# Optimization experiments

Measured on AMD Instinct MI355X. Metric: run time of the kernel, lower is better.

The kernel has to match this reference:

```python
import jax, jax.numpy as jnp
import numpy as np

COORD_DIM = 2
ENTITY_DIM = 1024
FIELD_DIM = 512
INPUT_DIM = 512
NUM_ENTITIES = 512
FIELD_RESOLUTION = 10000  # grid_size = 100


def _gelu(x):
    return jax.nn.gelu(x, approximate=False)  # torch nn.GELU default (erf)


def setup_inputs() -> dict:
    key = jax.random.key(0)
    ks = jax.random.split(key, 9)
    std = 0.02  # matches _init_parameters
    B, S = 8, 4096
    x = jax.random.normal(ks[0], (B, S, INPUT_DIM), dtype=jnp.float32)
    # DensityField: density_projection = Linear(D,F) GELU Linear(F,F) GELU; coordinate_generator = Linear(F,2)
    W1 = jax.random.normal(ks[1], (INPUT_DIM, FIELD_DIM), jnp.float32) * std
    b1 = jnp.zeros((FIELD_DIM,), jnp.float32)
    W2 = jax.random.normal(ks[2], (FIELD_DIM, FIELD_DIM), jnp.float32) * std
    b2 = jnp.zeros((FIELD_DIM,), jnp.float32)
    Wc = jax.random.normal(ks[3], (FIELD_DIM, COORD_DIM), jnp.float32) * std
    bc = jnp.zeros((COORD_DIM,), jnp.float32)
    # entity_mapper: Linear(F+2, F) GELU Linear(F, E+2+1)
    We1 = jax.random.normal(ks[4], (FIELD_DIM + COORD_DIM, FIELD_DIM), jnp.float32) * std
    be1 = jnp.zeros((FIELD_DIM,), jnp.float32)
    We2 = jax.random.normal(ks[5], (FIELD_DIM, ENTITY_DIM + COORD_DIM + 1), jnp.float32) * std
    be2 = jnp.zeros((ENTITY_DIM + COORD_DIM + 1,), jnp.float32)
    # output_projection: Linear(E, 2E) GELU Linear(2E, D)
    Wo1 = jax.random.normal(ks[6], (ENTITY_DIM, 2 * ENTITY_DIM), jnp.float32) * std
    bo1 = jnp.zeros((2 * ENTITY_DIM,), jnp.float32)
    Wo2 = jax.random.normal(ks[7], (2 * ENTITY_DIM, INPUT_DIM), jnp.float32) * std
    bo2 = jnp.zeros((INPUT_DIM,), jnp.float32)
    return dict(x=x, W1=W1, b1=b1, W2=W2, b2=b2, Wc=Wc, bc=bc,
                We1=We1, be1=be1, We2=We2, be2=be2,
                Wo1=Wo1, bo1=bo1, Wo2=Wo2, bo2=bo2)


def _forward(x, W1, b1, W2, b2, Wc, bc, We1, be1, We2, be2, Wo1, bo1, Wo2, bo2):
    # --- DensityField ---
    df = _gelu(_gelu(x @ W1 + b1) @ W2 + b2)          # [B,S,F]
    coords = df @ Wc + bc                              # [B,S,2]
    # --- ContinuousEntityExtractor ---
    field_input = jnp.concatenate([coords, df], axis=-1)          # [B,S,2+F]
    ef = _gelu(field_input @ We1 + be1) @ We2 + be2                # [B,S,E+3]
    importance = jnp.linalg.norm(ef, axis=-1)                      # [B,S]
    _, top_idx = jax.lax.top_k(importance, NUM_ENTITIES)           # [B,Ne]
    sel = jnp.take_along_axis(ef, top_idx[..., None], axis=1)     # [B,Ne,E+3]
    positions = sel[..., :COORD_DIM]                               # [B,Ne,2]
    states = sel[..., COORD_DIM:COORD_DIM + ENTITY_DIM]            # [B,Ne,E]
    # --- ContinuousOutputGenerator ---
    proj = _gelu(states @ Wo1 + bo1) @ Wo2 + bo2                   # [B,Ne,D]
    grid_size = int(FIELD_RESOLUTION ** 0.5)
    g = jnp.linspace(-1.0, 1.0, grid_size)
    gx, gy = jnp.meshgrid(g, g, indexing='ij')
    grid = jnp.stack([gx.ravel(), gy.ravel()], axis=-1)            # [G2,2]
    # squared euclidean distances via expansion (torch: cdist then **2)
    g2 = jnp.sum(grid * grid, axis=-1)                             # [G2]
    p2 = jnp.sum(positions * positions, axis=-1)                   # [B,Ne]
    gp = jnp.einsum('gc,bnc->bgn', grid, positions)                # [B,G2,Ne]
    sq = g2[None, :, None] + p2[:, None, :] - 2.0 * gp             # [B,G2,Ne]
    attn = jnp.exp(-sq / 0.1)
    attn = attn / (attn.sum(axis=-1, keepdims=True) + 1e-8)
    out = jnp.einsum('bgn,bnd->bgd', attn, proj)                   # [B,G2,D]
    return out


def reference(x, W1, b1, W2, b2, Wc, bc, We1, be1, We2, be2, Wo1, bo1, Wo2, bo2):
    return _forward(x, W1, b1, W2, b2, Wc, bc, We1, be1, We2, be2, Wo1, bo1, Wo2, bo2)
```

## Files before the change

kernel.cpp:

```cpp
#include <hip/hip_runtime.h>
#include <hip/hip_bf16.h>
#include <math.h>


typedef __attribute__((ext_vector_type(8))) short bf16x8;
typedef __attribute__((ext_vector_type(4))) float f32x4;

__device__ __forceinline__ float gelu_exact(float x) {
    return 0.5f * x * (1.0f + erff(x * 0.7071067811865476f));
}

__device__ __forceinline__ void async_copy16(const void* g, void* l) {
    __builtin_amdgcn_global_load_lds(
        (const __attribute__((address_space(1))) unsigned int*)g,
        (__attribute__((address_space(3))) unsigned int*)l, 16, 0, 0);
}

__global__ __launch_bounds__(256) void split_kernel(
    const float* __restrict__ in,
    __hip_bfloat16* __restrict__ hi, __hip_bfloat16* __restrict__ lo)
{
    const int i4 = blockIdx.x * 256 + threadIdx.x;
    const float4 v = ((const float4*)in)[i4];
    __hip_bfloat16 h0 = __float2bfloat16(v.x);
    __hip_bfloat16 h1 = __float2bfloat16(v.y);
    __hip_bfloat16 h2 = __float2bfloat16(v.z);
    __hip_bfloat16 h3 = __float2bfloat16(v.w);
    __hip_bfloat16 l0 = __float2bfloat16(v.x - __bfloat162float(h0));
    __hip_bfloat16 l1 = __float2bfloat16(v.y - __bfloat162float(h1));
    __hip_bfloat16 l2 = __float2bfloat16(v.z - __bfloat162float(h2));
    __hip_bfloat16 l3 = __float2bfloat16(v.w - __bfloat162float(h3));
    union { __hip_bfloat16 h[4]; short4 s; } uh, ul;
    uh.h[0] = h0; uh.h[1] = h1; uh.h[2] = h2; uh.h[3] = h3;
    ul.h[0] = l0; ul.h[1] = l1; ul.h[2] = l2; ul.h[3] = l3;
    ((short4*)hi)[i4] = uh.s;
    ((short4*)lo)[i4] = ul.s;
}

__global__ __launch_bounds__(256) void transpose_split_kernel(
    const float* __restrict__ in,
    __hip_bfloat16* __restrict__ outH, __hip_bfloat16* __restrict__ outL,
    int K, int N)
{
    __shared__ float tile[32][33];
    const int k0 = blockIdx.y * 32, n0 = blockIdx.x * 32;
    const int t = threadIdx.x;
    const int lr = t >> 5, lc = t & 31;
    #pragma unroll
    for (int p = 0; p < 4; p++) {
        const int r = p * 8 + lr;
        const int n = n0 + lc;
        tile[r][lc] = (n < N) ? in[(size_t)(k0 + r) * N + n] : 0.f;
    }
    __syncthreads();
    #pragma unroll
    for (int p = 0; p < 4; p++) {
        const int r = p * 8 + lr;
        const float v = tile[lc][r];
        const __hip_bfloat16 h = __float2bfloat16(v);
        const __hip_bfloat16 l = __float2bfloat16(v - __bfloat162float(h));
        outH[(size_t)(n0 + r) * K + k0 + lc] = h;
        outL[(size_t)(n0 + r) * K + k0 + lc] = l;
    }
}

__global__ __launch_bounds__(256) void init_kernel(
    float* __restrict__ IMP, float* __restrict__ CRD,
    const float* __restrict__ bc)
{
    const int t = blockIdx.x * 256 + threadIdx.x;
    IMP[t] = 0.f;
    ((float2*)CRD)[t] = make_float2(bc[0], bc[1]);
}

template<bool GELU, bool RANK2, bool EFMODE, bool FUSEC>
__global__ __launch_bounds__(256) void gemm3k(
    const __hip_bfloat16* __restrict__ Ahi, const __hip_bfloat16* __restrict__ Alo,
    const __hip_bfloat16* __restrict__ Bhi, const __hip_bfloat16* __restrict__ Blo,
    const float* __restrict__ bias,
    __hip_bfloat16* __restrict__ Chi, __hip_bfloat16* __restrict__ Clo,
    __hip_bfloat16* __restrict__ EFB, float* __restrict__ EFC,
    float* __restrict__ IMP,
    const float* __restrict__ A2, const float* __restrict__ W2r,
    float* __restrict__ CRD, const float* __restrict__ Wc)
{
    __shared__ __align__(16) __hip_bfloat16 AsH[4096];
    __shared__ __align__(16) __hip_bfloat16 AsL[4096];
    __shared__ __align__(16) __hip_bfloat16 BsH[4096];
    __shared__ __align__(16) __hip_bfloat16 BsL[4096];
    const int t = threadIdx.x;
    const int wave = t >> 6, lane = t & 63;
    const int wave_m = wave >> 1, wave_n = wave & 1;
    const int fr = lane & 15, quad = lane >> 4;
    const int gx = gridDim.x;
    const int L = blockIdx.y * gx + blockIdx.x;
    const int xcd = L & 7, kk_ = L >> 3;
    const int m_blk = xcd * (gridDim.y >> 3) + kk_ / gx;
    const int n_blk = kk_ % gx;
    const int m0 = m_blk * 128;
    const int n0 = n_blk * 128;
    const int lrow   = lane & 15;
    const int lchunk = (lane >> 4) * 8;

    f32x4 acc[4][4] = {};

    const int abase = wave_m * 2048 + quad * 128 + fr * 8;
    const int bbase = wave_n * 2048 + quad * 128 + fr * 8;

    for (int step = 0; step < 16; ++step) {
        const int kk = step << 5;
        #pragma unroll
        for (int s = 0; s < 2; s++) {
            const int seg = wave * 2 + s;
            const size_t ao = (size_t)(m0 + seg * 16 + lrow) * 512 + kk + lchunk;
            const size_t bo = (size_t)(n0 + seg * 16 + lrow) * 512 + kk + lchunk;
            async_copy16(Ahi + ao, &AsH[seg * 512]);
            async_copy16(Alo + ao, &AsL[seg * 512]);
            async_copy16(Bhi + bo, &BsH[seg * 512]);
            async_copy16(Blo + bo, &BsL[seg * 512]);
        }
        __syncthreads();
        bf16x8 ah[4], al[4], bh[4], bl[4];
        #pragma unroll
        for (int i = 0; i < 4; i++) {
            ah[i] = *(const bf16x8*)&AsH[abase + i * 512];
            al[i] = *(const bf16x8*)&AsL[abase + i * 512];
        }
        #pragma unroll
        for (int j = 0; j < 4; j++) {
            bh[j] = *(const bf16x8*)&BsH[bbase + j * 512];
            bl[j] = *(const bf16x8*)&BsL[bbase + j * 512];
        }
        #pragma unroll
        for (int i = 0; i < 4; i++)
            #pragma unroll
            for (int j = 0; j < 4; j++)
                acc[i][j] = __builtin_amdgcn_mfma_f32_16x16x32_bf16(
                    ah[i], bh[j], acc[i][j], 0, 0, 0);
        #pragma unroll
        for (int i = 0; i < 4; i++)
            #pragma unroll
            for (int j = 0; j < 4; j++)
                acc[i][j] = __builtin_amdgcn_mfma_f32_16x16x32_bf16(
                    ah[i], bl[j], acc[i][j], 0, 0, 0);
        #pragma unroll
        for (int i = 0; i < 4; i++)
            #pragma unroll
            for (int j = 0; j < 4; j++)
                acc[i][j] = __builtin_amdgcn_mfma_f32_16x16x32_bf16(
                    al[i], bh[j], acc[i][j], 0, 0, 0);
        __syncthreads();
    }

    #pragma unroll
    for (int i = 0; i < 4; i++) {
        const int gmb = m0 + wave_m * 64 + i * 16 + quad * 4;
        float a2x[4], a2y[4];
        if (RANK2) {
            #pragma unroll
            for (int r = 0; r < 4; r++) {
                a2x[r] = A2[(size_t)(gmb + r) * 2];
                a2y[r] = A2[(size_t)(gmb + r) * 2 + 1];
            }
        }
        float f0[4] = {0.f, 0.f, 0.f, 0.f};
        float f1[4] = {0.f, 0.f, 0.f, 0.f};
        #pragma unroll
        for (int j = 0; j < 4; j++) {
            const int gn = n0 + wave_n * 64 + j * 16 + fr;
            const bool nok = !EFMODE || (gn < 1027);
            const float bv = nok ? bias[gn] : 0.f;
            float w2a = 0.f, w2b = 0.f;
            if (RANK2) { w2a = W2r[gn]; w2b = W2r[512 + gn]; }
            float wcx = 0.f, wcy = 0.f;
            if (FUSEC) {
                const float2 wc = ((const float2*)Wc)[gn];
                wcx = wc.x; wcy = wc.y;
            }
            #pragma unroll
            for (int r = 0; r < 4; r++) {
                const int gm = gmb + r;
                float v = acc[i][j][r] + bv;
                if (RANK2) v += a2x[r] * w2a + a2y[r] * w2b;
                if (GELU) v = gelu_exact(v);
                if (EFMODE) {
                    if (gn < 2) EFC[(size_t)gm * 2 + gn] = v;
                    else if (gn < 1026)
                        EFB[(size_t)gm * 1024 + gn - 2] = __float2bfloat16(v);
                    if (nok) f0[r] += v * v;
                } else {
                    const __hip_bfloat16 h = __float2bfloat16(v);
                    const __hip_bfloat16 l =
                        __float2bfloat16(v - __bfloat162float(h));
                    Chi[(size_t)gm * 512 + gn] = h;
                    Clo[(size_t)gm * 512 + gn] = l;
                    if (FUSEC) { f0[r] += v * wcx; f1[r] += v * wcy; }
                }
            }
        }
        if (EFMODE || FUSEC) {
            #pragma unroll
            for (int r = 0; r < 4; r++) {
                float a = f0[r], b = f1[r];
                #pragma unroll
                for (int off = 1; off < 16; off <<= 1) {
                    a += __shfl_xor(a, off);
                    if (FUSEC) b += __shfl_xor(b, off);
                }
                if (fr == 0) {
                    if (FUSEC) {
                        atomicAdd(&CRD[(size_t)(gmb + r) * 2],     a);
                        atomicAdd(&CRD[(size_t)(gmb + r) * 2 + 1], b);
                    } else {
                        atomicAdd(&IMP[gmb + r], a);
                    }
                }
            }
        }
    }
}

__global__ __launch_bounds__(1024) void topk_kernel(
    const float* __restrict__ IMP, int* __restrict__ IDX)
{
    __shared__ float v[4096];
    __shared__ int   ix[4096];
    const int b = blockIdx.x, t = threadIdx.x;
    for (int i = t; i < 4096; i += 1024) {
        v[i] = sqrtf(IMP[b * 4096 + i]);
        ix[i] = i;
    }
    __syncthreads();
    for (int k = 2; k <= 4096; k <<= 1) {
        for (int j = k >> 1; j > 0; j >>= 1) {
            for (int q = 0; q < 4; q++) {
                const int i = t + (q << 10);
                const int l = i ^ j;
                if (l > i) {
                    const float vi = v[i], vl = v[l];
                    const int   ii = ix[i], il = ix[l];
                    const bool after = (vi < vl) || (vi == vl && ii > il);
                    const bool dirAsc = ((i & k) == 0);
                    if (dirAsc ? after : !after) {
                        v[i] = vl; v[l] = vi; ix[i] = il; ix[l] = ii;
                    }
                }
            }
            __syncthreads();
        }
    }
    if (t < 512) IDX[b * 512 + t] = ix[t];
}

__global__ __launch_bounds__(256) void gather_kernel(
    const __hip_bfloat16* __restrict__ EFB, const float* __restrict__ EFC,
    const int* __restrict__ IDX,
    float* __restrict__ POS, __hip_bfloat16* __restrict__ ST)
{
    const int bn  = blockIdx.x;
    const int b   = bn >> 9;
    const int row = IDX[bn];
    const size_t src = (size_t)(b * 4096) + row;
    const int t = threadIdx.x;
    if (t < 2) POS[(size_t)bn * 2 + t] = EFC[src * 2 + t];
    const unsigned int* s = (const unsigned int*)(EFB + src * 1024);
    unsigned int* d = (unsigned int*)(ST + (size_t)bn * 1024);
    d[t]       = s[t];
    d[t + 256] = s[t + 256];
}

__global__ __launch_bounds__(256) void transpose_cvt_kernel(
    const float* __restrict__ in, __hip_bfloat16* __restrict__ out,
    int K, int N)
{
    __shared__ float tile[32][33];
    const int k0 = blockIdx.y * 32, n0 = blockIdx.x * 32;
    const int t = threadIdx.x;
    const int lr = t >> 5, lc = t & 31;
    #pragma unroll
    for (int p = 0; p < 4; p++) {
        const int r = p * 8 + lr;
        tile[r][lc] = in[(size_t)(k0 + r) * N + n0 + lc];
    }
    __syncthreads();
    #pragma unroll
    for (int p = 0; p < 4; p++) {
        const int r = p * 8 + lr;
        out[(size_t)(n0 + r) * K + k0 + lc] = __float2bfloat16(tile[lc][r]);
    }
}

__global__ __launch_bounds__(256) void transpose_proj_kernel(
    const __hip_bfloat16* __restrict__ in, __hip_bfloat16* __restrict__ out)
{
    __shared__ __hip_bfloat16 tile[32][33];
    const int b = blockIdx.z;
    const int n0 = blockIdx.y * 32, d0 = blockIdx.x * 32;
    const int t = threadIdx.x;
    const int lr = t >> 5, lc = t & 31;
    #pragma unroll
    for (int p = 0; p < 4; p++) {
        const int r = p * 8 + lr;
        tile[r][lc] = in[((size_t)b * 512 + n0 + r) * 512 + d0 + lc];
    }
    __syncthreads();
    #pragma unroll
    for (int p = 0; p < 4; p++) {
        const int r = p * 8 + lr;
        out[((size_t)b * 512 + d0 + r) * 512 + n0 + lc] = tile[lc][r];
    }
}

template<bool GELU>
__global__ __launch_bounds__(256, 4) void gemm_post(
    const __hip_bfloat16* __restrict__ A,
    const __hip_bfloat16* __restrict__ BT,
    const float* __restrict__ bias,
    __hip_bfloat16* __restrict__ C,
    int N, int K)
{
    __shared__ __align__(16) __hip_bfloat16 As[2][128][32];
    __shared__ __align__(16) __hip_bfloat16 Bs[2][128][32];
    const int t = threadIdx.x;
    const int wave = t >> 6, lane = t & 63;
    const int wave_m = wave >> 1, wave_n = wave & 1;
    const int fr = lane & 15, quad = lane >> 4;
    const int gx = gridDim.x;
    const int nwg = gx * gridDim.y;
    int lid = blockIdx.y * gx + blockIdx.x;
    {
        const int chunk = nwg >> 3;
        lid = (lid & 7) * chunk + (lid >> 3);
    }
    const int m0 = (lid / gx) * 128;
    const int n0 = (lid % gx) * 128;
    const int srow = lane >> 2;
    const int skc  = (lane & 3) * 8;
    const int nsteps = K >> 5;

    f32x4 acc[4][4] = {};

    auto STAGE = [&](int buf, int step) {
        const int kk = step << 5;
        #pragma unroll
        for (int s = 0; s < 2; s++) {
            const int seg = wave * 2 + s;
            const int row = seg * 16 + srow;
            async_copy16(A  + (size_t)(m0 + row) * K + kk + skc,
                         &As[buf][seg * 16][0]);
            async_copy16(BT + (size_t)(n0 + row) * K + kk + skc,
                         &Bs[buf][seg * 16][0]);
        }
    };

    STAGE(0, 0);
    __syncthreads();
    int cur = 0;
    for (int step = 0; step < nsteps; ++step) {
        if (step + 1 < nsteps) STAGE(cur ^ 1, step + 1);
        bf16x8 af[4], bfv[4];
        #pragma unroll
        for (int i = 0; i < 4; i++)
            af[i] = *(const bf16x8*)&As[cur][wave_m * 64 + i * 16 + fr][quad * 8];
        #pragma unroll
        for (int j = 0; j < 4; j++)
            bfv[j] = *(const bf16x8*)&Bs[cur][wave_n * 64 + j * 16 + fr][quad * 8];
        #pragma unroll
        for (int i = 0; i < 4; i++)
            #pragma unroll
            for (int j = 0; j < 4; j++)
                acc[i][j] = __builtin_amdgcn_mfma_f32_16x16x32_bf16(
                    af[i], bfv[j], acc[i][j], 0, 0, 0);
        __syncthreads();
        cur ^= 1;
    }
    #pragma unroll
    for (int i = 0; i < 4; i++) {
        const int gm = m0 + wave_m * 64 + i * 16 + quad * 4;
        #pragma unroll
        for (int j = 0; j < 4; j++) {
            const int gn = n0 + wave_n * 64 + j * 16 + fr;
            const float bv = bias[gn];
            #pragma unroll
            for (int r = 0; r < 4; r++) {
                float v = acc[i][j][r] + bv;
                if (GELU) v = gelu_exact(v);
                C[(size_t)(gm + r) * N + gn] = __float2bfloat16(v);
            }
        }
    }
}

__global__ __launch_bounds__(256) void attn_mfma_kernel(
    const float* __restrict__ POS,
    const __hip_bfloat16* __restrict__ PROJT,
    float* __restrict__ OUT)
{
    __shared__ __align__(16) __hip_bfloat16 Bs[256][32];
    __shared__ float2 pos_s[512];
    __shared__ float srow_s[4][16];
    const int t = threadIdx.x;
    const int wave = t >> 6, lane = t & 63;
    const int fr = lane & 15, quad = lane >> 4;
    const int b  = blockIdx.z;
    const int g0 = blockIdx.x * 64;
    const int d0 = blockIdx.y * 256;

    {
        const float2* p = (const float2*)(POS + (size_t)b * 512 * 2);
        pos_s[t]       = p[t];
        pos_s[256 + t] = p[256 + t];
    }
    const int g = g0 + wave * 16 + fr;
    const bool gv = g < 10000;
    const float step = 2.0f / 99.0f;
    const int gi = gv ? (g / 100) : 0;
    const int gj = gv ? (g - gi * 100) : 0;
    const float gx = -1.f + step * (float)gi;
    const float gy = -1.f + step * (float)gj;

    f32x4 acc[16] = {};
    float wsum = 0.f;
    __syncthreads();

    for (int n0 = 0; n0 < 512; n0 += 32) {
        #pragma unroll
        for (int s = 0; s < 4; s++) {
            const int seg = wave * 4 + s;
            const __hip_bfloat16* gB = PROJT
                + ((size_t)b * 512 + d0 + seg * 16 + (lane >> 2)) * 512
                + n0 + (lane & 3) * 8;
            async_copy16(gB, &Bs[seg * 16][0]);
        }
        bf16x8 wf;
        float wl = 0.f;
        #pragma unroll
        for (int j = 0; j < 8; j++) {
            const int n = n0 + quad * 8 + j;
            const float2 pn = pos_s[n];
            const float dx = gx - pn.x, dy = gy - pn.y;
            const float w = gv ? __expf(-10.0f * (dx * dx + dy * dy)) : 0.f;
            const __hip_bfloat16 wb = __float2bfloat16(w);
            union { __hip_bfloat16 h; short s; } u; u.h = wb;
            wf[j] = u.s;
            wl += __bfloat162float(wb);
        }
        wsum += wl;
        __syncthreads();
        #pragma unroll
        for (int j = 0; j < 16; j++) {
            const bf16x8 bv = *(const bf16x8*)&Bs[j * 16 + fr][quad * 8];
            acc[j] = __builtin_amdgcn_mfma_f32_16x16x32_bf16(wf, bv, acc[j], 0, 0, 0);
        }
        __syncthreads();
    }
    wsum += __shfl_xor(wsum, 16);
    wsum += __shfl_xor(wsum, 32);
    if (lane < 16) srow_s[wave][lane] = wsum;
    __syncthreads();
    const int rbase = quad * 4;
    float inv[4];
    #pragma unroll
    for (int r = 0; r < 4; r++)
        inv[r] = 1.0f / (srow_s[wave][rbase + r] + 1e-8f);
    #pragma unroll
    for (int j = 0; j < 16; j++) {
        const int col = d0 + j * 16 + fr;
        #pragma unroll
        for (int r = 0; r < 4; r++) {
            const int gr = g0 + wave * 16 + rbase + r;
            if (gr < 10000)
                OUT[((size_t)b * 10000 + gr) * 512 + col] = acc[j][r] * inv[r];
        }
    }
}

extern "C" void kernel_launch(void* const* d_in, const int* in_sizes, int n_in,
                              void* d_out, int out_size, void* d_ws, size_t ws_size,
                              hipStream_t stream)
{
    const float* x   = (const float*)d_in[0];
    const float* W1  = (const float*)d_in[1];
    const float* b1  = (const float*)d_in[2];
    const float* W2  = (const float*)d_in[3];
    const float* b2  = (const float*)d_in[4];
    const float* Wc  = (const float*)d_in[5];
    const float* bc  = (const float*)d_in[6];
    const float* We1 = (const float*)d_in[7];
    const float* be1 = (const float*)d_in[8];
    const float* We2 = (const float*)d_in[9];
    const float* be2 = (const float*)d_in[10];
    const float* Wo1 = (const float*)d_in[11];
    const float* bo1 = (const float*)d_in[12];
    const float* Wo2 = (const float*)d_in[13];
    const float* bo2 = (const float*)d_in[14];
    float* out = (float*)d_out;

    const size_t BS = 32768;
    const size_t ACT = BS * 512;
    __hip_bfloat16* P0h = (__hip_bfloat16*)d_ws;
    __hip_bfloat16* P0l = P0h + ACT;
    __hip_bfloat16* P1h = P0l + ACT;
    __hip_bfloat16* P1l = P1h + ACT;
    __hip_bfloat16* EFB = P1l + ACT;
    float* EFC = (float*)(EFB + BS * 1024);
    float* CRD = EFC + BS * 2;
    float* IMP = CRD + BS * 2;
    int*   IDX = (int*)(IMP + BS);
    float* POS = (float*)(IDX + 4096);
    __hip_bfloat16* W1Th = (__hip_bfloat16*)(POS + 4096 * 2);
    __hip_bfloat16* W1Tl = W1Th + 512 * 512;
    __hip_bfloat16* W2Th = W1Tl + 512 * 512;
    __hip_bfloat16* W2Tl = W2Th + 512 * 512;
    __hip_bfloat16* We1Th = W2Tl + 512 * 512;
    __hip_bfloat16* We1Tl = We1Th + 512 * 512;
    __hip_bfloat16* We2Th = We1Tl + 512 * 512;
    __hip_bfloat16* We2Tl = We2Th + (size_t)1152 * 512;
    __hip_bfloat16* ST    = P0h;
    __hip_bfloat16* H4    = ST + (size_t)4096 * 1024;
    __hip_bfloat16* PROJ  = H4 + (size_t)4096 * 2048;
    __hip_bfloat16* PROJT = PROJ + (size_t)4096 * 512;
    __hip_bfloat16* Wo1T  = PROJT + (size_t)4096 * 512;
    __hip_bfloat16* Wo2T  = Wo1T + (size_t)2048 * 1024;

    dim3 blk(256);
    split_kernel<<<dim3(16384), blk, 0, stream>>>(x, P0h, P0l);
    transpose_split_kernel<<<dim3(16, 16), blk, 0, stream>>>(W1, W1Th, W1Tl, 512, 512);
    transpose_split_kernel<<<dim3(16, 16), blk, 0, stream>>>(W2, W2Th, W2Tl, 512, 512);
    transpose_split_kernel<<<dim3(16, 16), blk, 0, stream>>>(We1 + 2 * 512, We1Th, We1Tl, 512, 512);
    transpose_split_kernel<<<dim3(36, 16), blk, 0, stream>>>(We2, We2Th, We2Tl, 512, 1027);
    init_kernel<<<dim3(128), blk, 0, stream>>>(IMP, CRD, bc);
    gemm3k<true, false, false, false><<<dim3(4, 256), blk, 0, stream>>>(
        P0h, P0l, W1Th, W1Tl, b1, P1h, P1l,
        nullptr, nullptr, nullptr, nullptr, nullptr, nullptr, nullptr);
    gemm3k<true, false, false, true><<<dim3(4, 256), blk, 0, stream>>>(
        P1h, P1l, W2Th, W2Tl, b2, P0h, P0l,
        nullptr, nullptr, nullptr, nullptr, nullptr, CRD, Wc);
    gemm3k<true, true, false, false><<<dim3(4, 256), blk, 0, stream>>>(
        P0h, P0l, We1Th, We1Tl, be1, P1h, P1l,
        nullptr, nullptr, nullptr, CRD, We1, nullptr, nullptr);
    gemm3k<false, false, true, false><<<dim3(9, 256), blk, 0, stream>>>(
        P1h, P1l, We2Th, We2Tl, be2, nullptr, nullptr,
        EFB, EFC, IMP, nullptr, nullptr, nullptr, nullptr);
    topk_kernel<<<dim3(8), dim3(1024), 0, stream>>>(IMP, IDX);
    transpose_cvt_kernel<<<dim3(64, 32), blk, 0, stream>>>(Wo1, Wo1T, 1024, 2048);
    transpose_cvt_kernel<<<dim3(16, 64), blk, 0, stream>>>(Wo2, Wo2T, 2048, 512);
    gather_kernel<<<dim3(4096), blk, 0, stream>>>(EFB, EFC, IDX, POS, ST);
    gemm_post<true><<<dim3(16, 32), blk, 0, stream>>>(
        ST, Wo1T, bo1, H4, 2048, 1024);
    gemm_post<false><<<dim3(4, 32), blk, 0, stream>>>(
        H4, Wo2T, bo2, PROJ, 512, 2048);
    transpose_proj_kernel<<<dim3(16, 16, 8), blk, 0, stream>>>(PROJ, PROJT);
    attn_mfma_kernel<<<dim3(157, 2, 8), blk, 0, stream>>>(POS, PROJT, out);
}
```

Before: 941.9 us.

## Restructure GEMM kernels: drop XCD swizzle, store EF as fp32, split wrappers

Turns the templated GEMM into a device body with one named wrapper kernel per stage, and replaces the XCD-aware block remapping with a plain blockIdx mapping. The shared-memory staging moves to a row-major [128][32] tile with a different lane-to-row load pattern. The entity-feature output is now stored as a full fp32 1027-wide row instead of split bf16/fp32 buffers, and the gather kernel converts to bf16 itself. This doubles the EF write traffic. The row-major LDS reads may also cause bank conflicts, and dropping the swizzle loses L2 locality, so the change looks more like a simplification than a speedup.

```diff
diff --git a/kernel.cpp b/kernel.cpp
--- a/kernel.cpp
+++ b/kernel.cpp
@@ -73,63 +73,56 @@
     ((float2*)CRD)[t] = make_float2(bc[0], bc[1]);
 }
 
-template<bool GELU, bool RANK2, bool EFMODE, bool FUSEC>
-__global__ __launch_bounds__(256) void gemm3k(
+template<bool GELU, bool RANK2, bool SPLIT, bool FUSEC, bool FUSEI>
+__device__ __forceinline__ void gemm3k_body(
     const __hip_bfloat16* __restrict__ Ahi, const __hip_bfloat16* __restrict__ Alo,
     const __hip_bfloat16* __restrict__ Bhi, const __hip_bfloat16* __restrict__ Blo,
     const float* __restrict__ bias,
+    float* __restrict__ Cf, int ldc,
     __hip_bfloat16* __restrict__ Chi, __hip_bfloat16* __restrict__ Clo,
-    __hip_bfloat16* __restrict__ EFB, float* __restrict__ EFC,
-    float* __restrict__ IMP,
+    int N,
     const float* __restrict__ A2, const float* __restrict__ W2r,
-    float* __restrict__ CRD, const float* __restrict__ Wc)
-{
-    __shared__ __align__(16) __hip_bfloat16 AsH[4096];
-    __shared__ __align__(16) __hip_bfloat16 AsL[4096];
-    __shared__ __align__(16) __hip_bfloat16 BsH[4096];
-    __shared__ __align__(16) __hip_bfloat16 BsL[4096];
+    float* __restrict__ CRD, const float* __restrict__ Wc,
+    float* __restrict__ IMP)
+{
+    __shared__ __align__(16) __hip_bfloat16 AsH[128][32];
+    __shared__ __align__(16) __hip_bfloat16 AsL[128][32];
+    __shared__ __align__(16) __hip_bfloat16 BsH[128][32];
+    __shared__ __align__(16) __hip_bfloat16 BsL[128][32];
     const int t = threadIdx.x;
     const int wave = t >> 6, lane = t & 63;
     const int wave_m = wave >> 1, wave_n = wave & 1;
     const int fr = lane & 15, quad = lane >> 4;
-    const int gx = gridDim.x;
-    const int L = blockIdx.y * gx + blockIdx.x;
-    const int xcd = L & 7, kk_ = L >> 3;
-    const int m_blk = xcd * (gridDim.y >> 3) + kk_ / gx;
-    const int n_blk = kk_ % gx;
-    const int m0 = m_blk * 128;
-    const int n0 = n_blk * 128;
-    const int lrow   = lane & 15;
-    const int lchunk = (lane >> 4) * 8;
+    const int m0 = blockIdx.y * 128;
+    const int n0 = blockIdx.x * 128;
+    const int srow = lane >> 2;
+    const int skc  = (lane & 3) * 8;
 
     f32x4 acc[4][4] = {};
 
-    const int abase = wave_m * 2048 + quad * 128 + fr * 8;
-    const int bbase = wave_n * 2048 + quad * 128 + fr * 8;
-
-    for (int step = 0; step < 16; ++step) {
-        const int kk = step << 5;
+    for (int k0 = 0; k0 < 512; k0 += 32) {
         #pragma unroll
         for (int s = 0; s < 2; s++) {
             const int seg = wave * 2 + s;
-            const size_t ao = (size_t)(m0 + seg * 16 + lrow) * 512 + kk + lchunk;
-            const size_t bo = (size_t)(n0 + seg * 16 + lrow) * 512 + kk + lchunk;
-            async_copy16(Ahi + ao, &AsH[seg * 512]);
-            async_copy16(Alo + ao, &AsL[seg * 512]);
-            async_copy16(Bhi + bo, &BsH[seg * 512]);
-            async_copy16(Blo + bo, &BsL[seg * 512]);
+            const int row = seg * 16 + srow;
+            const size_t ao = (size_t)(m0 + row) * 512 + k0 + skc;
+            const size_t bo = (size_t)(n0 + row) * 512 + k0 + skc;
+            async_copy16(Ahi + ao, &AsH[seg * 16][0]);
+            async_copy16(Alo + ao, &AsL[seg * 16][0]);
+            async_copy16(Bhi + bo, &BsH[seg * 16][0]);
+            async_copy16(Blo + bo, &BsL[seg * 16][0]);
         }
         __syncthreads();
         bf16x8 ah[4], al[4], bh[4], bl[4];
         #pragma unroll
         for (int i = 0; i < 4; i++) {
-            ah[i] = *(const bf16x8*)&AsH[abase + i * 512];
-            al[i] = *(const bf16x8*)&AsL[abase + i * 512];
+            ah[i] = *(const bf16x8*)&AsH[wave_m * 64 + i * 16 + fr][quad * 8];
+            al[i] = *(const bf16x8*)&AsL[wave_m * 64 + i * 16 + fr][quad * 8];
         }
         #pragma unroll
         for (int j = 0; j < 4; j++) {
-            bh[j] = *(const bf16x8*)&BsH[bbase + j * 512];
-            bl[j] = *(const bf16x8*)&BsL[bbase + j * 512];
+            bh[j] = *(const bf16x8*)&BsH[wave_n * 64 + j * 16 + fr][quad * 8];
+            bl[j] = *(const bf16x8*)&BsL[wave_n * 64 + j * 16 + fr][quad * 8];
         }
         #pragma unroll
         for (int i = 0; i < 4; i++)
@@ -168,7 +161,7 @@
         #pragma unroll
         for (int j = 0; j < 4; j++) {
             const int gn = n0 + wave_n * 64 + j * 16 + fr;
-            const bool nok = !EFMODE || (gn < 1027);
+            const bool nok = SPLIT || (gn < N);
             const float bv = nok ? bias[gn] : 0.f;
             float w2a = 0.f, w2b = 0.f;
             if (RANK2) { w2a = W2r[gn]; w2b = W2r[512 + gn]; }
@@ -183,22 +176,20 @@
                 float v = acc[i][j][r] + bv;
                 if (RANK2) v += a2x[r] * w2a + a2y[r] * w2b;
                 if (GELU) v = gelu_exact(v);
-                if (EFMODE) {
-                    if (gn < 2) EFC[(size_t)gm * 2 + gn] = v;
-                    else if (gn < 1026)
-                        EFB[(size_t)gm * 1024 + gn - 2] = __float2bfloat16(v);
-                    if (nok) f0[r] += v * v;
-                } else {
+                if (SPLIT) {
                     const __hip_bfloat16 h = __float2bfloat16(v);
                     const __hip_bfloat16 l =
                         __float2bfloat16(v - __bfloat162float(h));
                     Chi[(size_t)gm * 512 + gn] = h;
                     Clo[(size_t)gm * 512 + gn] = l;
-                    if (FUSEC) { f0[r] += v * wcx; f1[r] += v * wcy; }
+                } else if (nok) {
+                    Cf[(size_t)gm * ldc + gn] = v;
                 }
+                if (FUSEC) { f0[r] += v * wcx; f1[r] += v * wcy; }
+                if (FUSEI && nok) f0[r] += v * v;
             }
         }
-        if (EFMODE || FUSEC) {
+        if (FUSEC || FUSEI) {
             #pragma unroll
             for (int r = 0; r < 4; r++) {
                 float a = f0[r], b = f1[r];
@@ -220,6 +211,52 @@
     }
 }
 
+__global__ __launch_bounds__(256) void gemm_h1(
+    const __hip_bfloat16* __restrict__ Ahi, const __hip_bfloat16* __restrict__ Alo,
+    const __hip_bfloat16* __restrict__ Bhi, const __hip_bfloat16* __restrict__ Blo,
+    const float* __restrict__ bias,
+    __hip_bfloat16* __restrict__ Chi, __hip_bfloat16* __restrict__ Clo)
+{
+    gemm3k_body<true, false, true, false, false>(
+        Ahi, Alo, Bhi, Blo, bias, nullptr, 0, Chi, Clo, 512,
+        nullptr, nullptr, nullptr, nullptr, nullptr);
+}
+
+__global__ __launch_bounds__(256) void gemm_df(
+    const __hip_bfloat16* __restrict__ Ahi, const __hip_bfloat16* __restrict__ Alo,
+    const __hip_bfloat16* __restrict__ Bhi, const __hip_bfloat16* __restrict__ Blo,
+    const float* __restrict__ bias,
+    __hip_bfloat16* __restrict__ Chi, __hip_bfloat16* __restrict__ Clo,
+    float* __restrict__ CRD, const float* __restrict__ Wc)
+{
+    gemm3k_body<true, false, true, true, false>(
+        Ahi, Alo, Bhi, Blo, bias, nullptr, 0, Chi, Clo, 512,
+        nullptr, nullptr, CRD, Wc, nullptr);
+}
+
+__global__ __launch_bounds__(256) void gemm_h3(
+    const __hip_bfloat16* __restrict__ Ahi, const __hip_bfloat16* __restrict__ Alo,
+    const __hip_bfloat16* __restrict__ Bhi, const __hip_bfloat16* __restrict__ Blo,
+    const float* __restrict__ bias,
+    __hip_bfloat16* __restrict__ Chi, __hip_bfloat16* __restrict__ Clo,
+    const float* __restrict__ A2, const float* __restrict__ W2r)
+{
+    gemm3k_body<true, true, true, false, false>(
+        Ahi, Alo, Bhi, Blo, bias, nullptr, 0, Chi, Clo, 512,
+        A2, W2r, nullptr, nullptr, nullptr);
+}
+
+__global__ __launch_bounds__(256) void gemm_ef(
+    const __hip_bfloat16* __restrict__ Ahi, const __hip_bfloat16* __restrict__ Alo,
+    const __hip_bfloat16* __restrict__ Bhi, const __hip_bfloat16* __restrict__ Blo,
+    const float* __restrict__ bias,
+    float* __restrict__ Cf, float* __restrict__ IMP)
+{
+    gemm3k_body<false, false, false, false, true>(
+        Ahi, Alo, Bhi, Blo, bias, Cf, 1027, nullptr, nullptr, 1027,
+        nullptr, nullptr, nullptr, nullptr, IMP);
+}
+
 __global__ __launch_bounds__(1024) void topk_kernel(
     const float* __restrict__ IMP, int* __restrict__ IDX)
 {
@@ -253,20 +290,17 @@
 }
 
 __global__ __launch_bounds__(256) void gather_kernel(
-    const __hip_bfloat16* __restrict__ EFB, const float* __restrict__ EFC,
-    const int* __restrict__ IDX,
+    const float* __restrict__ EF, const int* __restrict__ IDX,
     float* __restrict__ POS, __hip_bfloat16* __restrict__ ST)
 {
     const int bn  = blockIdx.x;
     const int b   = bn >> 9;
     const int row = IDX[bn];
-    const size_t src = (size_t)(b * 4096) + row;
-    const int t = threadIdx.x;
-    if (t < 2) POS[(size_t)bn * 2 + t] = EFC[src * 2 + t];
-    const unsigned int* s = (const unsigned int*)(EFB + src * 1024);
-    unsigned int* d = (unsigned int*)(ST + (size_t)bn * 1024);
-    d[t]       = s[t];
-    d[t + 256] = s[t + 256];
+    const float* src = EF + ((size_t)(b * 4096) + row) * 1027;
+    const int t = threadIdx.x;
+    if (t < 2) POS[(size_t)bn * 2 + t] = src[t];
+    __hip_bfloat16* dst = ST + (size_t)bn * 1024;
+    for (int k = t; k < 1024; k += 256) dst[k] = __float2bfloat16(src[2 + k]);
 }
 
 __global__ __launch_bounds__(256) void transpose_cvt_kernel(
@@ -312,7 +346,7 @@
 }
 
 template<bool GELU>
-__global__ __launch_bounds__(256, 4) void gemm_post(
+__device__ __forceinline__ void gemm_post_body(
     const __hip_bfloat16* __restrict__ A,
     const __hip_bfloat16* __restrict__ BT,
     const float* __restrict__ bias,
@@ -389,6 +423,22 @@
             }
         }
     }
+}
+
+__global__ __launch_bounds__(256, 4) void gemm_o1(
+    const __hip_bfloat16* __restrict__ A, const __hip_bfloat16* __restrict__ BT,
+    const float* __restrict__ bias, __hip_bfloat16* __restrict__ C,
+    int N, int K)
+{
+    gemm_post_body<true>(A, BT, bias, C, N, K);
+}
+
+__global__ __launch_bounds__(256, 4) void gemm_o2(
+    const __hip_bfloat16* __restrict__ A, const __hip_bfloat16* __restrict__ BT,
+    const float* __restrict__ bias, __hip_bfloat16* __restrict__ C,
+    int N, int K)
+{
+    gemm_post_body<false>(A, BT, bias, C, N, K);
 }
 
 __global__ __launch_bounds__(256) void attn_mfma_kernel(
@@ -502,9 +552,8 @@
     __hip_bfloat16* P0l = P0h + ACT;
     __hip_bfloat16* P1h = P0l + ACT;
     __hip_bfloat16* P1l = P1h + ACT;
-    __hip_bfloat16* EFB = P1l + ACT;
-    float* EFC = (float*)(EFB + BS * 1024);
-    float* CRD = EFC + BS * 2;
+    float* EF  = (float*)(P1l + ACT);
+    float* CRD = EF + BS * 1027;
     float* IMP = CRD + BS * 2;
     int*   IDX = (int*)(IMP + BS);
     float* POS = (float*)(IDX + 4096);
@@ -530,26 +579,20 @@
     transpose_split_kernel<<<dim3(16, 16), blk, 0, stream>>>(We1 + 2 * 512, We1Th, We1Tl, 512, 512);
     transpose_split_kernel<<<dim3(36, 16), blk, 0, stream>>>(We2, We2Th, We2Tl, 512, 1027);
     init_kernel<<<dim3(128), blk, 0, stream>>>(IMP, CRD, bc);
-    gemm3k<true, false, false, false><<<dim3(4, 256), blk, 0, stream>>>(
-        P0h, P0l, W1Th, W1Tl, b1, P1h, P1l,
-        nullptr, nullptr, nullptr, nullptr, nullptr, nullptr, nullptr);
-    gemm3k<true, false, false, true><<<dim3(4, 256), blk, 0, stream>>>(
-        P1h, P1l, W2Th, W2Tl, b2, P0h, P0l,
-        nullptr, nullptr, nullptr, nullptr, nullptr, CRD, Wc);
-    gemm3k<true, true, false, false><<<dim3(4, 256), blk, 0, stream>>>(
-        P0h, P0l, We1Th, We1Tl, be1, P1h, P1l,
-        nullptr, nullptr, nullptr, CRD, We1, nullptr, nullptr);
-    gemm3k<false, false, true, false><<<dim3(9, 256), blk, 0, stream>>>(
-        P1h, P1l, We2Th, We2Tl, be2, nullptr, nullptr,
-        EFB, EFC, IMP, nullptr, nullptr, nullptr, nullptr);
+    gemm_h1<<<dim3(4, 256), blk, 0, stream>>>(
+        P0h, P0l, W1Th, W1Tl, b1, P1h, P1l);
+    gemm_df<<<dim3(4, 256), blk, 0, stream>>>(
+        P1h, P1l, W2Th, W2Tl, b2, P0h, P0l, CRD, Wc);
+    gemm_h3<<<dim3(4, 256), blk, 0, stream>>>(
+        P0h, P0l, We1Th, We1Tl, be1, P1h, P1l, CRD, We1);
+    gemm_ef<<<dim3(9, 256), blk, 0, stream>>>(
+        P1h, P1l, We2Th, We2Tl, be2, EF, IMP);
     topk_kernel<<<dim3(8), dim3(1024), 0, stream>>>(IMP, IDX);
     transpose_cvt_kernel<<<dim3(64, 32), blk, 0, stream>>>(Wo1, Wo1T, 1024, 2048);
     transpose_cvt_kernel<<<dim3(16, 64), blk, 0, stream>>>(Wo2, Wo2T, 2048, 512);
-    gather_kernel<<<dim3(4096), blk, 0, stream>>>(EFB, EFC, IDX, POS, ST);
-    gemm_post<true><<<dim3(16, 32), blk, 0, stream>>>(
-        ST, Wo1T, bo1, H4, 2048, 1024);
-    gemm_post<false><<<dim3(4, 32), blk, 0, stream>>>(
-        H4, Wo2T, bo2, PROJ, 512, 2048);
+    gather_kernel<<<dim3(4096), blk, 0, stream>>>(EF, IDX, POS, ST);
+    gemm_o1<<<dim3(16, 32), blk, 0, stream>>>(ST, Wo1T, bo1, H4, 2048, 1024);
+    gemm_o2<<<dim3(4, 32), blk, 0, stream>>>(H4, Wo2T, bo2, PROJ, 512, 2048);
     transpose_proj_kernel<<<dim3(16, 16, 8), blk, 0, stream>>>(PROJ, PROJT);
     attn_mfma_kernel<<<dim3(157, 2, 8), blk, 0, stream>>>(POS, PROJT, out);
 }
```

Result: no change. 925.2 us (-1.8%).
